# Optimization experiments

Measured on AMD Instinct MI355X. Metric: run time of the kernel, lower is better.

## Reference

```python
import jax, jax.numpy as jnp
import numpy as np

H = 512  # hidden_size


def _highway_lstm(x, lengths, Wi, bi, Ws, bs):
    B, T, D = x.shape
    # Precompute all input projections in one big GEMM: [B, T, 6H]
    pi = jnp.einsum('btd,kd->btk', x, Wi) + bi
    mask = jnp.arange(T)[None, :] < lengths[:, None]  # [B, T]

    def step(carry, inp):
        h, c = carry
        pi_t, m = inp                      # pi_t: [B, 6H], m: [B]
        ps = h @ Ws.T + bs                 # [B, 5H]
        i = jax.nn.sigmoid(pi_t[:, 0*H:1*H] + ps[:, 0*H:1*H])
        f = jax.nn.sigmoid(pi_t[:, 1*H:2*H] + ps[:, 1*H:2*H])
        g = jnp.tanh(pi_t[:, 2*H:3*H] + ps[:, 2*H:3*H])
        o = jax.nn.sigmoid(pi_t[:, 3*H:4*H] + ps[:, 3*H:4*H])
        c_new = i * g + f * c
        out = o * jnp.tanh(c_new)
        # highway gate blends LSTM output with linear input projection
        r = jax.nn.sigmoid(pi_t[:, 4*H:5*H] + ps[:, 4*H:5*H])
        out = r * out + (1.0 - r) * pi_t[:, 5*H:6*H]
        m2 = m[:, None]
        h_new = jnp.where(m2, out, h)      # hold state past sequence end
        c_new = jnp.where(m2, c_new, c)
        y = jnp.where(m2, out, jnp.zeros_like(out))  # packed-seq padding = 0
        return (h_new, c_new), y

    h0 = jnp.zeros((B, H), x.dtype)
    c0 = jnp.zeros((B, H), x.dtype)
    (hT, cT), ys = jax.lax.scan(step, (h0, c0),
                                (jnp.swapaxes(pi, 0, 1), mask.T))
    return jnp.swapaxes(ys, 0, 1), hT, cT  # outputs [B,T,H], final (h, c)


def setup_inputs() -> dict:
    key = jax.random.key(0)
    ks = jax.random.split(key, 4)
    B, T, D = 32, 512, 512
    x = jax.random.normal(ks[0], (B, T, D), dtype=jnp.float32)
    lengths = jax.random.randint(ks[1], (B,), 1, T + 1, dtype=jnp.int32)
    Wi = jax.random.normal(ks[2], (6 * H, D), dtype=jnp.float32) * 0.05
    bi = jnp.zeros((6 * H,), dtype=jnp.float32)
    Ws = jax.random.normal(ks[3], (5 * H, H), dtype=jnp.float32) * 0.05
    bs = jnp.zeros((5 * H,), dtype=jnp.float32)
    return {"x": x, "lengths": lengths, "Wi": Wi, "bi": bi, "Ws": Ws, "bs": bs}


def reference(x, lengths, Wi, bi, Ws, bs):
    return _highway_lstm(x, lengths, Wi, bi, Ws, bs)
```

## Files before the change

kernel.cpp:

```cpp
#include <hip/hip_runtime.h>
#include <stdint.h>

typedef __attribute__((ext_vector_type(8))) short short8;
typedef __attribute__((ext_vector_type(4))) float f32x4;
typedef unsigned long long u64;

constexpr int cB = 32, cT = 512, cD = 512, cH = 512;
constexpr int cKI = 6 * cH;
constexpr int NWG = 32;
constexpr int THR = 320;
constexpr int LDW = 40;
constexpr int HP  = 520;
constexpr int RNG = 3;

__device__ __forceinline__ float bf2f(unsigned short u) {
  union { unsigned int i; float f; } x; x.i = ((unsigned int)u) << 16; return x.f;
}
__device__ __forceinline__ unsigned short f2bf(float f) {
  union { float f; unsigned int i; } x; x.f = f;
  return (unsigned short)((x.i + 0x7fffu + ((x.i >> 16) & 1u)) >> 16);
}
__device__ __forceinline__ float sigm(float v) { return 1.0f / (1.0f + __expf(-v)); }
__device__ __forceinline__ float tanh_f(float v) { return 2.0f / (1.0f + __expf(-2.0f * v)) - 1.0f; }

__global__ __launch_bounds__(256) void gemm_pi(
    const float* __restrict__ x,
    const float* __restrict__ Wi,
    const float* __restrict__ bi,
    unsigned short* __restrict__ pi)
{
  __shared__ __align__(16) unsigned short Ai[128 * LDW];
  __shared__ __align__(16) unsigned short Bi[128 * LDW];

  const int tid = threadIdx.x;
  const int lane = tid & 63;
  const int w = tid >> 6;
  const int wm = w & 1, wn = w >> 1;
  const int k0 = blockIdx.x * 128;
  const int n0 = blockIdx.y * 128;

  f32x4 acc[4][4];
  #pragma unroll
  for (int i = 0; i < 4; i++)
    #pragma unroll
    for (int j = 0; j < 4; j++) acc[i][j] = (f32x4){0.f, 0.f, 0.f, 0.f};

  for (int kk = 0; kk < cD; kk += 32) {
    __syncthreads();
    #pragma unroll
    for (int it = 0; it < 4; it++) {
      int idx = tid + it * 256;
      int r = idx >> 3, ch = idx & 7;
      int na = n0 + r;
      int bb = na & 31, tt = na >> 5;
      float4 va = *(const float4*)(x + ((size_t)bb * cT + tt) * cD + kk + ch * 4);
      ushort4 pa; pa.x = f2bf(va.x); pa.y = f2bf(va.y); pa.z = f2bf(va.z); pa.w = f2bf(va.w);
      *(ushort4*)(Ai + r * LDW + ch * 4) = pa;
      float4 vb = *(const float4*)(Wi + (size_t)(k0 + r) * cD + kk + ch * 4);
      ushort4 pb; pb.x = f2bf(vb.x); pb.y = f2bf(vb.y); pb.z = f2bf(vb.z); pb.w = f2bf(vb.w);
      *(ushort4*)(Bi + r * LDW + ch * 4) = pb;
    }
    __syncthreads();

    short8 af[4], bfr[4];
    const int q = lane >> 4;
    #pragma unroll
    for (int mi = 0; mi < 4; mi++) {
      int m = wm * 64 + mi * 16 + (lane & 15);
      af[mi] = *(const short8*)(Ai + m * LDW + q * 8);
    }
    #pragma unroll
    for (int ni = 0; ni < 4; ni++) {
      int n = wn * 64 + ni * 16 + (lane & 15);
      bfr[ni] = *(const short8*)(Bi + n * LDW + q * 8);
    }
    #pragma unroll
    for (int mi = 0; mi < 4; mi++)
      #pragma unroll
      for (int ni = 0; ni < 4; ni++)
        acc[mi][ni] = __builtin_amdgcn_mfma_f32_16x16x32_bf16(af[mi], bfr[ni], acc[mi][ni], 0, 0, 0);
  }

  #pragma unroll
  for (int ni = 0; ni < 4; ni++) {
    int kl = wn * 64 + ni * 16 + (lane & 15);
    float bv = bi[k0 + kl];
    #pragma unroll
    for (int mi = 0; mi < 4; mi++) {
      int nl = wm * 64 + mi * 16 + (lane >> 4) * 4;
      int nb = n0 + nl;
      int b0 = nb & 31, tt = nb >> 5;
      f32x4 a = acc[mi][ni];
      unsigned short v0 = f2bf(a.x + bv), v1 = f2bf(a.y + bv);
      unsigned short v2 = f2bf(a.z + bv), v3 = f2bf(a.w + bv);
      uint2 pv; pv.x = (unsigned)v0 | ((unsigned)v1 << 16);
      pv.y = (unsigned)v2 | ((unsigned)v3 << 16);
      *(uint2*)(pi + ((size_t)tt * cKI + k0 + kl) * cB + b0) = pv;
    }
  }
}

__global__ __launch_bounds__(THR, 1) void lstm_rec(
    const unsigned short* __restrict__ pi,
    const float* __restrict__ Ws,
    const float* __restrict__ bs,
    const int* __restrict__ lengths,
    unsigned short* __restrict__ hbuf,
    int* __restrict__ bar,
    float* __restrict__ out)
{
  __shared__ __align__(16) unsigned short ws_lds[80 * HP];
  __shared__ __align__(16) unsigned short h_lds[32 * HP];
  __shared__ __align__(16) unsigned short piL[RNG * 6 * 16 * 32];
  __shared__ __align__(16) float ps_lds[5 * 16 * 36];
  __shared__ __align__(16) float c_lds[16 * 32];
  __shared__ __align__(16) unsigned short hstg[16 * 32];
  __shared__ float bs_lds[80];
  __shared__ int len_lds[32];

  const int tid = threadIdx.x;
  const int lane = tid & 63;
  const int w = tid >> 6;
  const int wg = blockIdx.x;
  const int ci0 = wg * 16;

  for (int q = tid; q < 80 * 128; q += THR) {
    int r = q >> 7, ch = q & 127;
    int grow = (r >> 4) * cH + ci0 + (r & 15);
    float4 v = *(const float4*)(Ws + (size_t)grow * cH + ch * 4);
    ushort4 p; p.x = f2bf(v.x); p.y = f2bf(v.y); p.z = f2bf(v.z); p.w = f2bf(v.w);
    *(ushort4*)(ws_lds + r * HP + ch * 4) = p;
  }
  if (tid < 80) bs_lds[tid] = bs[(tid >> 4) * cH + ci0 + (tid & 15)];
  if (tid < cB) len_lds[tid] = lengths[tid];
  for (int q = tid; q < 16 * 32; q += THR) c_lds[q] = 0.0f;
  for (int q = tid; q < 32 * HP / 4; q += THR) ((u64*)h_lds)[q] = 0ull;

  for (int s = 0; s < 2; s++) {
    const unsigned short* pit = pi + (size_t)s * cKI * cB;
    for (int j = tid; j < 384; j += THR) {
      int g = j >> 6, rem = j & 63, c = rem >> 2, q = rem & 3;
      uint4 v = *(const uint4*)(pit + ((size_t)g * cH + ci0 + c) * cB + q * 8);
      *(uint4*)(piL + s * 3072 + (g * 16 + c) * 32 + q * 8) = v;
    }
  }
  __syncthreads();

  int target = NWG;
  const int mc = lane & 15;
  const int kq = lane >> 4;
  const int brow = w * 16 + mc;

  for (int t = 0; t < cT; t++) {
    u64 hv[13];
    if (t > 0) {
      u64* hs = (u64*)(hbuf + (size_t)(t & 1) * cB * cH);
      #pragma unroll
      for (int k = 0; k < 13; k++) {
        int idx = tid + k * THR;
        if (idx < 4096)
          hv[k] = __hip_atomic_load(hs + idx, __ATOMIC_RELAXED, __HIP_MEMORY_SCOPE_AGENT);
      }
    }
    uint4 pv0, pv1;
    const bool pf = (t + 2) < cT;
    const int slot_w = (t + 2) % RNG;
    if (pf) {
      const unsigned short* pit = pi + (size_t)(t + 2) * cKI * cB;
      { int g = tid >> 6, rem = tid & 63, c = rem >> 2, q = rem & 3;
        pv0 = *(const uint4*)(pit + ((size_t)g * cH + ci0 + c) * cB + q * 8); }
      int j1 = tid + THR;
      if (j1 < 384) { int g = j1 >> 6, rem = j1 & 63, c = rem >> 2, q = rem & 3;
        pv1 = *(const uint4*)(pit + ((size_t)g * cH + ci0 + c) * cB + q * 8); }
    }
    if (t > 0) {
      #pragma unroll
      for (int k = 0; k < 13; k++) {
        int idx = tid + k * THR;
        if (idx < 4096) {
          int b = idx >> 7, ch = idx & 127;
          *(u64*)(h_lds + b * HP + ch * 4) = hv[k];
        }
      }
    }
    __syncthreads();

    f32x4 acc0 = (f32x4){0.f,0.f,0.f,0.f}, acc1 = (f32x4){0.f,0.f,0.f,0.f};
    #pragma unroll
    for (int kt = 0; kt < 16; kt++) {
      int kc = kt * 4 + kq;
      short8 a0 = *(const short8*)(h_lds + mc * HP + kc * 8);
      short8 a1 = *(const short8*)(h_lds + (16 + mc) * HP + kc * 8);
      short8 bb = *(const short8*)(ws_lds + brow * HP + kc * 8);
      acc0 = __builtin_amdgcn_mfma_f32_16x16x32_bf16(a0, bb, acc0, 0, 0, 0);
      acc1 = __builtin_amdgcn_mfma_f32_16x16x32_bf16(a1, bb, acc1, 0, 0, 0);
    }
    {
      int r0 = kq * 4;
      *(f32x4*)(ps_lds + (w * 16 + mc) * 36 + r0) = acc0;
      *(f32x4*)(ps_lds + (w * 16 + mc) * 36 + r0 + 16) = acc1;
    }
    if (pf) {
      { int g = tid >> 6, rem = tid & 63, c = rem >> 2, q = rem & 3;
        *(uint4*)(piL + slot_w * 3072 + (g * 16 + c) * 32 + q * 8) = pv0; }
      int j1 = tid + THR;
      if (j1 < 384) { int g = j1 >> 6, rem = j1 & 63, c = rem >> 2, q = rem & 3;
        *(uint4*)(piL + slot_w * 3072 + (g * 16 + c) * 32 + q * 8) = pv1; }
    }
    __syncthreads();

    const unsigned short* pl = piL + (t % RNG) * 3072;
    #pragma unroll
    for (int u = 0; u < 2; u++) {
      int idx = tid + u * THR;
      if (idx < 512) {
        int b = idx & 31, c = idx >> 5;
        int col = ci0 + c;
        float a_i = bf2f(pl[(0*16 + c)*32 + b]) + ps_lds[(0*16 + c)*36 + b] + bs_lds[0*16 + c];
        float a_f = bf2f(pl[(1*16 + c)*32 + b]) + ps_lds[(1*16 + c)*36 + b] + bs_lds[1*16 + c];
        float a_g = bf2f(pl[(2*16 + c)*32 + b]) + ps_lds[(2*16 + c)*36 + b] + bs_lds[2*16 + c];
        float a_o = bf2f(pl[(3*16 + c)*32 + b]) + ps_lds[(3*16 + c)*36 + b] + bs_lds[3*16 + c];
        float a_r = bf2f(pl[(4*16 + c)*32 + b]) + ps_lds[(4*16 + c)*36 + b] + bs_lds[4*16 + c];
        float p5  = bf2f(pl[(5*16 + c)*32 + b]);
        float gi = sigm(a_i), gf = sigm(a_f), gg = tanh_f(a_g), go = sigm(a_o), gr = sigm(a_r);
        float cold = c_lds[c * 32 + b];
        float cn = gi * gg + gf * cold;
        float ov = go * tanh_f(cn);
        ov = gr * ov + (1.0f - gr) * p5;
        bool m = (t < len_lds[b]);
        float hold = bf2f(h_lds[b * HP + col]);
        float hn = m ? ov : hold;
        c_lds[c * 32 + b] = m ? cn : cold;
        hstg[c * 32 + b] = f2bf(hn);
        out[((size_t)b * cT + t) * cH + col] = m ? ov : 0.0f;
        if (t == cT - 1)
          out[(size_t)cB * cT * cH + (size_t)b * cH + col] = hn;
      }
    }
    __syncthreads();
    if (tid < 128) {
      int b = tid >> 2, q = tid & 3;
      u64 pk = (u64)hstg[(q*4 + 0)*32 + b] | ((u64)hstg[(q*4 + 1)*32 + b] << 16)
             | ((u64)hstg[(q*4 + 2)*32 + b] << 32) | ((u64)hstg[(q*4 + 3)*32 + b] << 48);
      u64* hd = (u64*)(hbuf + (size_t)((t + 1) & 1) * cB * cH);
      __hip_atomic_store(hd + b * 128 + (ci0 >> 2) + q, pk, __ATOMIC_RELAXED, __HIP_MEMORY_SCOPE_AGENT);
    }
    __syncthreads();
    if (tid == 0) {
      __hip_atomic_fetch_add(bar, 1, __ATOMIC_RELAXED, __HIP_MEMORY_SCOPE_AGENT);
      while (__hip_atomic_load(bar, __ATOMIC_RELAXED, __HIP_MEMORY_SCOPE_AGENT) < target)
        __builtin_amdgcn_s_sleep(1);
    }
    target += NWG;
    __syncthreads();
  }

  #pragma unroll
  for (int u = 0; u < 2; u++) {
    int idx = tid + u * THR;
    if (idx < 512) {
      int b = idx & 31, c = idx >> 5;
      out[(size_t)cB * cT * cH + (size_t)cB * cH + (size_t)b * cH + ci0 + c] = c_lds[c * 32 + b];
    }
  }
}

extern "C" void kernel_launch(void* const* d_in, const int* in_sizes, int n_in,
                              void* d_out, int out_size, void* d_ws, size_t ws_size,
                              hipStream_t stream) {
  const float* x       = (const float*)d_in[0];
  const int* lengths   = (const int*)d_in[1];
  const float* Wi      = (const float*)d_in[2];
  const float* bi      = (const float*)d_in[3];
  const float* Ws      = (const float*)d_in[4];
  const float* bs      = (const float*)d_in[5];
  float* out = (float*)d_out;

  char* ws = (char*)d_ws;
  int* bar = (int*)ws;
  unsigned short* hbuf = (unsigned short*)(ws + 512);
  unsigned short* pi   = (unsigned short*)(ws + (1 << 20));

  hipMemsetAsync(bar, 0, 256, stream);
  dim3 grid1(cKI / 128, (cB * cT) / 128);
  gemm_pi<<<grid1, 256, 0, stream>>>(x, Wi, bi, pi);
  lstm_rec<<<NWG, THR, 0, stream>>>(pi, Ws, bs, lengths, hbuf, bar, out);
}
```

Before: 2.165 ms.

## Keep recurrent weights in registers, read h directly, use per-workgroup flag barrier

Each wave now keeps its slice of Ws as bf16 MFMA B-fragments in registers instead of LDS. The hidden state is loaded from global memory straight into A-operand registers, with no LDS staging pass and no separate pack-and-store step. The grid-wide atomic counter barrier is replaced by per-workgroup step flags that 32 lanes poll with a wave vote, and h is written with scalar 16-bit atomic stores. This removes LDS round trips and a sync per step, but raises register pressure (64 u64 plus 16 short8) and makes each workgroup issue many small uncoalesced global loads and stores per step.

```diff
diff --git a/kernel.cpp b/kernel.cpp
--- a/kernel.cpp
+++ b/kernel.cpp
@@ -10,7 +10,6 @@
 constexpr int NWG = 32;
 constexpr int THR = 320;
 constexpr int LDW = 40;
-constexpr int HP  = 520;
 constexpr int RNG = 3;
 
 __device__ __forceinline__ float bf2f(unsigned short u) {
@@ -106,11 +105,9 @@
     const float* __restrict__ bs,
     const int* __restrict__ lengths,
     unsigned short* __restrict__ hbuf,
-    int* __restrict__ bar,
+    int* __restrict__ flags,
     float* __restrict__ out)
 {
-  __shared__ __align__(16) unsigned short ws_lds[80 * HP];
-  __shared__ __align__(16) unsigned short h_lds[32 * HP];
   __shared__ __align__(16) unsigned short piL[RNG * 6 * 16 * 32];
   __shared__ __align__(16) float ps_lds[5 * 16 * 36];
   __shared__ __align__(16) float c_lds[16 * 32];
@@ -123,18 +120,27 @@
   const int w = tid >> 6;
   const int wg = blockIdx.x;
   const int ci0 = wg * 16;
-
-  for (int q = tid; q < 80 * 128; q += THR) {
-    int r = q >> 7, ch = q & 127;
-    int grow = (r >> 4) * cH + ci0 + (r & 15);
-    float4 v = *(const float4*)(Ws + (size_t)grow * cH + ch * 4);
-    ushort4 p; p.x = f2bf(v.x); p.y = f2bf(v.y); p.z = f2bf(v.z); p.w = f2bf(v.w);
-    *(ushort4*)(ws_lds + r * HP + ch * 4) = p;
+  const int mc = lane & 15;
+  const int kq = lane >> 4;
+
+  short8 bfrag[16];
+  {
+    const float* wsrow = Ws + (size_t)(w * cH + ci0 + mc) * cH;
+    #pragma unroll
+    for (int kt = 0; kt < 16; kt++) {
+      float4 f0 = *(const float4*)(wsrow + kt * 32 + kq * 8);
+      float4 f1 = *(const float4*)(wsrow + kt * 32 + kq * 8 + 4);
+      short8 pk;
+      pk[0] = (short)f2bf(f0.x); pk[1] = (short)f2bf(f0.y);
+      pk[2] = (short)f2bf(f0.z); pk[3] = (short)f2bf(f0.w);
+      pk[4] = (short)f2bf(f1.x); pk[5] = (short)f2bf(f1.y);
+      pk[6] = (short)f2bf(f1.z); pk[7] = (short)f2bf(f1.w);
+      bfrag[kt] = pk;
+    }
   }
   if (tid < 80) bs_lds[tid] = bs[(tid >> 4) * cH + ci0 + (tid & 15)];
   if (tid < cB) len_lds[tid] = lengths[tid];
-  for (int q = tid; q < 16 * 32; q += THR) c_lds[q] = 0.0f;
-  for (int q = tid; q < 32 * HP / 4; q += THR) ((u64*)h_lds)[q] = 0ull;
+  for (int q = tid; q < 16 * 32; q += THR) { c_lds[q] = 0.0f; hstg[q] = 0; }
 
   for (int s = 0; s < 2; s++) {
     const unsigned short* pit = pi + (size_t)s * cKI * cB;
@@ -144,24 +150,23 @@
       *(uint4*)(piL + s * 3072 + (g * 16 + c) * 32 + q * 8) = v;
     }
   }
+  if (tid < 128) {
+    int b = tid >> 2, q = tid & 3;
+    u64* hd0 = (u64*)hbuf;
+    __hip_atomic_store(hd0 + b * 128 + (ci0 >> 2) + q, 0ull, __ATOMIC_RELAXED, __HIP_MEMORY_SCOPE_AGENT);
+  }
   __syncthreads();
-
-  int target = NWG;
-  const int mc = lane & 15;
-  const int kq = lane >> 4;
-  const int brow = w * 16 + mc;
+  if (tid == 0)
+    __hip_atomic_store(&flags[wg], 1, __ATOMIC_RELAXED, __HIP_MEMORY_SCOPE_AGENT);
+  if (tid < 32) {
+    while (true) {
+      int f = __hip_atomic_load(&flags[tid], __ATOMIC_RELAXED, __HIP_MEMORY_SCOPE_AGENT);
+      if (__all(f >= 1)) break;
+    }
+  }
+  __syncthreads();
 
   for (int t = 0; t < cT; t++) {
-    u64 hv[13];
-    if (t > 0) {
-      u64* hs = (u64*)(hbuf + (size_t)(t & 1) * cB * cH);
-      #pragma unroll
-      for (int k = 0; k < 13; k++) {
-        int idx = tid + k * THR;
-        if (idx < 4096)
-          hv[k] = __hip_atomic_load(hs + idx, __ATOMIC_RELAXED, __HIP_MEMORY_SCOPE_AGENT);
-      }
-    }
     uint4 pv0, pv1;
     const bool pf = (t + 2) < cT;
     const int slot_w = (t + 2) % RNG;
@@ -173,27 +178,25 @@
       if (j1 < 384) { int g = j1 >> 6, rem = j1 & 63, c = rem >> 2, q = rem & 3;
         pv1 = *(const uint4*)(pit + ((size_t)g * cH + ci0 + c) * cB + q * 8); }
     }
-    if (t > 0) {
-      #pragma unroll
-      for (int k = 0; k < 13; k++) {
-        int idx = tid + k * THR;
-        if (idx < 4096) {
-          int b = idx >> 7, ch = idx & 127;
-          *(u64*)(h_lds + b * HP + ch * 4) = hv[k];
-        }
-      }
-    }
-    __syncthreads();
-
+    const unsigned short* hsrc = hbuf + (size_t)(t & 1) * cB * cH;
+    u64 av[64];
+    #pragma unroll
+    for (int kt = 0; kt < 16; kt++) {
+      const u64* p0 = (const u64*)(hsrc + mc * cH + kt * 32 + kq * 8);
+      const u64* p1 = (const u64*)(hsrc + (16 + mc) * cH + kt * 32 + kq * 8);
+      av[kt*4+0] = __hip_atomic_load(p0,     __ATOMIC_RELAXED, __HIP_MEMORY_SCOPE_AGENT);
+      av[kt*4+1] = __hip_atomic_load(p0 + 1, __ATOMIC_RELAXED, __HIP_MEMORY_SCOPE_AGENT);
+      av[kt*4+2] = __hip_atomic_load(p1,     __ATOMIC_RELAXED, __HIP_MEMORY_SCOPE_AGENT);
+      av[kt*4+3] = __hip_atomic_load(p1 + 1, __ATOMIC_RELAXED, __HIP_MEMORY_SCOPE_AGENT);
+    }
     f32x4 acc0 = (f32x4){0.f,0.f,0.f,0.f}, acc1 = (f32x4){0.f,0.f,0.f,0.f};
     #pragma unroll
     for (int kt = 0; kt < 16; kt++) {
-      int kc = kt * 4 + kq;
-      short8 a0 = *(const short8*)(h_lds + mc * HP + kc * 8);
-      short8 a1 = *(const short8*)(h_lds + (16 + mc) * HP + kc * 8);
-      short8 bb = *(const short8*)(ws_lds + brow * HP + kc * 8);
-      acc0 = __builtin_amdgcn_mfma_f32_16x16x32_bf16(a0, bb, acc0, 0, 0, 0);
-      acc1 = __builtin_amdgcn_mfma_f32_16x16x32_bf16(a1, bb, acc1, 0, 0, 0);
+      union { u64 q[2]; short8 s; } ua0, ua1;
+      ua0.q[0] = av[kt*4+0]; ua0.q[1] = av[kt*4+1];
+      ua1.q[0] = av[kt*4+2]; ua1.q[1] = av[kt*4+3];
+      acc0 = __builtin_amdgcn_mfma_f32_16x16x32_bf16(ua0.s, bfrag[kt], acc0, 0, 0, 0);
+      acc1 = __builtin_amdgcn_mfma_f32_16x16x32_bf16(ua1.s, bfrag[kt], acc1, 0, 0, 0);
     }
     {
       int r0 = kq * 4;
@@ -210,6 +213,7 @@
     __syncthreads();
 
     const unsigned short* pl = piL + (t % RNG) * 3072;
+    unsigned short* hdst = hbuf + (size_t)((t + 1) & 1) * cB * cH;
     #pragma unroll
     for (int u = 0; u < 2; u++) {
       int idx = tid + u * THR;
@@ -228,31 +232,30 @@
         float ov = go * tanh_f(cn);
         ov = gr * ov + (1.0f - gr) * p5;
         bool m = (t < len_lds[b]);
-        float hold = bf2f(h_lds[b * HP + col]);
+        float hold = bf2f(hstg[c * 32 + b]);
         float hn = m ? ov : hold;
         c_lds[c * 32 + b] = m ? cn : cold;
-        hstg[c * 32 + b] = f2bf(hn);
+        unsigned short hb = f2bf(hn);
+        hstg[c * 32 + b] = hb;
         out[((size_t)b * cT + t) * cH + col] = m ? ov : 0.0f;
         if (t == cT - 1)
           out[(size_t)cB * cT * cH + (size_t)b * cH + col] = hn;
+        else
+          __hip_atomic_store(&hdst[b * cH + col], hb, __ATOMIC_RELAXED, __HIP_MEMORY_SCOPE_AGENT);
       }
     }
-    __syncthreads();
-    if (tid < 128) {
-      int b = tid >> 2, q = tid & 3;
-      u64 pk = (u64)hstg[(q*4 + 0)*32 + b] | ((u64)hstg[(q*4 + 1)*32 + b] << 16)
-             | ((u64)hstg[(q*4 + 2)*32 + b] << 32) | ((u64)hstg[(q*4 + 3)*32 + b] << 48);
-      u64* hd = (u64*)(hbuf + (size_t)((t + 1) & 1) * cB * cH);
-      __hip_atomic_store(hd + b * 128 + (ci0 >> 2) + q, pk, __ATOMIC_RELAXED, __HIP_MEMORY_SCOPE_AGENT);
-    }
-    __syncthreads();
-    if (tid == 0) {
-      __hip_atomic_fetch_add(bar, 1, __ATOMIC_RELAXED, __HIP_MEMORY_SCOPE_AGENT);
-      while (__hip_atomic_load(bar, __ATOMIC_RELAXED, __HIP_MEMORY_SCOPE_AGENT) < target)
-        __builtin_amdgcn_s_sleep(1);
-    }
-    target += NWG;
-    __syncthreads();
+    if (t + 1 < cT) {
+      __syncthreads();
+      if (tid == 0)
+        __hip_atomic_store(&flags[wg], t + 2, __ATOMIC_RELAXED, __HIP_MEMORY_SCOPE_AGENT);
+      if (tid < 32) {
+        while (true) {
+          int f = __hip_atomic_load(&flags[tid], __ATOMIC_RELAXED, __HIP_MEMORY_SCOPE_AGENT);
+          if (__all(f >= t + 2)) break;
+        }
+      }
+      __syncthreads();
+    }
   }
 
   #pragma unroll
@@ -277,12 +280,12 @@
   float* out = (float*)d_out;
 
   char* ws = (char*)d_ws;
-  int* bar = (int*)ws;
+  int* flags = (int*)ws;
   unsigned short* hbuf = (unsigned short*)(ws + 512);
   unsigned short* pi   = (unsigned short*)(ws + (1 << 20));
 
-  hipMemsetAsync(bar, 0, 256, stream);
+  hipMemsetAsync(flags, 0, 256, stream);
   dim3 grid1(cKI / 128, (cB * cT) / 128);
   gemm_pi<<<grid1, 256, 0, stream>>>(x, Wi, bi, pi);
-  lstm_rec<<<NWG, THR, 0, stream>>>(pi, Ws, bs, lengths, hbuf, bar, out);
-}
+  lstm_rec<<<NWG, THR, 0, stream>>>(pi, Ws, bs, lengths, hbuf, flags, out);
+}
```

New measurement: 6.253 ms. 189% more time.

## Replace atomic counter barrier with per-block flags and keep Ws in registers

Applied to the files above, without the earlier changes.

Replaces the single shared atomic-counter grid barrier with per-workgroup padded flag words that 32 lanes poll together, removing fetch_add contention on one counter and the sleep in the spin loop. Recurrent weight fragments are now held in registers (16 short8 per lane) instead of being read from LDS every step, which cuts LDS traffic and frees about 83KB of LDS. The barrier is skipped after the last timestep, and hbuf is zeroed on device behind an initial flag handshake. This raises register pressure, and the polling relies on relaxed atomics with no explicit fences.

```diff
diff --git a/kernel.cpp b/kernel.cpp
--- a/kernel.cpp
+++ b/kernel.cpp
@@ -12,6 +12,7 @@
 constexpr int LDW = 40;
 constexpr int HP  = 520;
 constexpr int RNG = 3;
+constexpr int FPAD = 16;
 
 __device__ __forceinline__ float bf2f(unsigned short u) {
   union { unsigned int i; float f; } x; x.i = ((unsigned int)u) << 16; return x.f;
@@ -106,10 +107,9 @@
     const float* __restrict__ bs,
     const int* __restrict__ lengths,
     unsigned short* __restrict__ hbuf,
-    int* __restrict__ bar,
+    int* __restrict__ flags,
     float* __restrict__ out)
 {
-  __shared__ __align__(16) unsigned short ws_lds[80 * HP];
   __shared__ __align__(16) unsigned short h_lds[32 * HP];
   __shared__ __align__(16) unsigned short piL[RNG * 6 * 16 * 32];
   __shared__ __align__(16) float ps_lds[5 * 16 * 36];
@@ -123,13 +123,23 @@
   const int w = tid >> 6;
   const int wg = blockIdx.x;
   const int ci0 = wg * 16;
-
-  for (int q = tid; q < 80 * 128; q += THR) {
-    int r = q >> 7, ch = q & 127;
-    int grow = (r >> 4) * cH + ci0 + (r & 15);
-    float4 v = *(const float4*)(Ws + (size_t)grow * cH + ch * 4);
-    ushort4 p; p.x = f2bf(v.x); p.y = f2bf(v.y); p.z = f2bf(v.z); p.w = f2bf(v.w);
-    *(ushort4*)(ws_lds + r * HP + ch * 4) = p;
+  const int mc = lane & 15;
+  const int kq = lane >> 4;
+
+  short8 bfrag[16];
+  {
+    const float* wsrow = Ws + (size_t)(w * cH + ci0 + mc) * cH;
+    #pragma unroll
+    for (int kt = 0; kt < 16; kt++) {
+      float4 f0 = *(const float4*)(wsrow + kt * 32 + kq * 8);
+      float4 f1 = *(const float4*)(wsrow + kt * 32 + kq * 8 + 4);
+      short8 pk;
+      pk[0] = (short)f2bf(f0.x); pk[1] = (short)f2bf(f0.y);
+      pk[2] = (short)f2bf(f0.z); pk[3] = (short)f2bf(f0.w);
+      pk[4] = (short)f2bf(f1.x); pk[5] = (short)f2bf(f1.y);
+      pk[6] = (short)f2bf(f1.z); pk[7] = (short)f2bf(f1.w);
+      bfrag[kt] = pk;
+    }
   }
   if (tid < 80) bs_lds[tid] = bs[(tid >> 4) * cH + ci0 + (tid & 15)];
   if (tid < cB) len_lds[tid] = lengths[tid];
@@ -144,12 +154,21 @@
       *(uint4*)(piL + s * 3072 + (g * 16 + c) * 32 + q * 8) = v;
     }
   }
+  if (tid < 128) {
+    int b = tid >> 2, q = tid & 3;
+    u64* hd0 = (u64*)hbuf;
+    __hip_atomic_store(hd0 + b * 128 + (ci0 >> 2) + q, 0ull, __ATOMIC_RELAXED, __HIP_MEMORY_SCOPE_AGENT);
+  }
   __syncthreads();
-
-  int target = NWG;
-  const int mc = lane & 15;
-  const int kq = lane >> 4;
-  const int brow = w * 16 + mc;
+  if (tid == 0)
+    __hip_atomic_store(&flags[wg * FPAD], 1, __ATOMIC_RELAXED, __HIP_MEMORY_SCOPE_AGENT);
+  if (tid < 32) {
+    while (true) {
+      int f = __hip_atomic_load(&flags[tid * FPAD], __ATOMIC_RELAXED, __HIP_MEMORY_SCOPE_AGENT);
+      if (__all(f >= 1)) break;
+    }
+  }
+  __syncthreads();
 
   for (int t = 0; t < cT; t++) {
     u64 hv[13];
@@ -191,9 +210,8 @@
       int kc = kt * 4 + kq;
       short8 a0 = *(const short8*)(h_lds + mc * HP + kc * 8);
       short8 a1 = *(const short8*)(h_lds + (16 + mc) * HP + kc * 8);
-      short8 bb = *(const short8*)(ws_lds + brow * HP + kc * 8);
-      acc0 = __builtin_amdgcn_mfma_f32_16x16x32_bf16(a0, bb, acc0, 0, 0, 0);
-      acc1 = __builtin_amdgcn_mfma_f32_16x16x32_bf16(a1, bb, acc1, 0, 0, 0);
+      acc0 = __builtin_amdgcn_mfma_f32_16x16x32_bf16(a0, bfrag[kt], acc0, 0, 0, 0);
+      acc1 = __builtin_amdgcn_mfma_f32_16x16x32_bf16(a1, bfrag[kt], acc1, 0, 0, 0);
     }
     {
       int r0 = kq * 4;
@@ -237,22 +255,26 @@
           out[(size_t)cB * cT * cH + (size_t)b * cH + col] = hn;
       }
     }
-    __syncthreads();
-    if (tid < 128) {
-      int b = tid >> 2, q = tid & 3;
-      u64 pk = (u64)hstg[(q*4 + 0)*32 + b] | ((u64)hstg[(q*4 + 1)*32 + b] << 16)
-             | ((u64)hstg[(q*4 + 2)*32 + b] << 32) | ((u64)hstg[(q*4 + 3)*32 + b] << 48);
-      u64* hd = (u64*)(hbuf + (size_t)((t + 1) & 1) * cB * cH);
-      __hip_atomic_store(hd + b * 128 + (ci0 >> 2) + q, pk, __ATOMIC_RELAXED, __HIP_MEMORY_SCOPE_AGENT);
-    }
-    __syncthreads();
-    if (tid == 0) {
-      __hip_atomic_fetch_add(bar, 1, __ATOMIC_RELAXED, __HIP_MEMORY_SCOPE_AGENT);
-      while (__hip_atomic_load(bar, __ATOMIC_RELAXED, __HIP_MEMORY_SCOPE_AGENT) < target)
-        __builtin_amdgcn_s_sleep(1);
-    }
-    target += NWG;
-    __syncthreads();
+    if (t + 1 < cT) {
+      __syncthreads();
+      if (tid < 128) {
+        int b = tid >> 2, q = tid & 3;
+        u64 pk = (u64)hstg[(q*4 + 0)*32 + b] | ((u64)hstg[(q*4 + 1)*32 + b] << 16)
+               | ((u64)hstg[(q*4 + 2)*32 + b] << 32) | ((u64)hstg[(q*4 + 3)*32 + b] << 48);
+        u64* hd = (u64*)(hbuf + (size_t)((t + 1) & 1) * cB * cH);
+        __hip_atomic_store(hd + b * 128 + (ci0 >> 2) + q, pk, __ATOMIC_RELAXED, __HIP_MEMORY_SCOPE_AGENT);
+      }
+      __syncthreads();
+      if (tid == 0)
+        __hip_atomic_store(&flags[wg * FPAD], t + 2, __ATOMIC_RELAXED, __HIP_MEMORY_SCOPE_AGENT);
+      if (tid < 32) {
+        while (true) {
+          int f = __hip_atomic_load(&flags[tid * FPAD], __ATOMIC_RELAXED, __HIP_MEMORY_SCOPE_AGENT);
+          if (__all(f >= t + 2)) break;
+        }
+      }
+      __syncthreads();
+    }
   }
 
   #pragma unroll
@@ -277,12 +299,12 @@
   float* out = (float*)d_out;
 
   char* ws = (char*)d_ws;
-  int* bar = (int*)ws;
-  unsigned short* hbuf = (unsigned short*)(ws + 512);
+  int* flags = (int*)ws;
+  unsigned short* hbuf = (unsigned short*)(ws + 4096);
   unsigned short* pi   = (unsigned short*)(ws + (1 << 20));
 
-  hipMemsetAsync(bar, 0, 256, stream);
+  hipMemsetAsync(flags, 0, NWG * FPAD * sizeof(int), stream);
   dim3 grid1(cKI / 128, (cB * cT) / 128);
   gemm_pi<<<grid1, 256, 0, stream>>>(x, Wi, bi, pi);
-  lstm_rec<<<NWG, THR, 0, stream>>>(pi, Ws, bs, lengths, hbuf, bar, out);
-}
+  lstm_rec<<<NWG, THR, 0, stream>>>(pi, Ws, bs, lengths, hbuf, flags, out);
+}
```

After: 2.002 ms. 1.08x faster.
